# Optimization experiments

Measured on AMD Instinct MI355X. Metric: run time of the kernel, lower is better.

Reference implementation:

```python
import jax, jax.numpy as jnp
import numpy as np

# ---- static configuration (mirrors init_kwargs) ----
B, NCAM = 1, 6
FC, FH, FW = 128, 16, 44              # featureShape
ORFH, ORFW = 128, 352                 # transformedImgShape H, W
D_ST, D_END, D_STEP = 1.0, 49.0, 1.0
D = int(np.arange(D_ST, D_END, D_STEP).shape[0])   # 48 depth bins
OUTC = 128
XB = (-50.0, 50.0, 1.0)
YB = (-50.0, 50.0, 1.0)
BEV_H = int((YB[1] - YB[0]) / YB[2])  # 100
BEV_W = int((XB[1] - XB[0]) / XB[2])  # 100
THRESH = 0.05                         # opacity_filter
ERR_TOL = 1.0                         # error_tolerance
COV_DILATE = 0.3                      # 3DGS low-pass on 2D cov diagonal
ALPHA_MAX = 0.99
ALPHA_MIN = 1.0 / 255.0
BN_EPS = 1e-3


def _frustum():
    ds = jnp.arange(D_ST, D_END, D_STEP, dtype=jnp.float32)[:, None, None]
    xs = jnp.linspace(0.0, ORFW - 1.0, FW, dtype=jnp.float32)[None, None, :]
    ys = jnp.linspace(0.0, ORFH - 1.0, FH, dtype=jnp.float32)[None, :, None]
    shp = (D, FH, FW)
    return jnp.stack([jnp.broadcast_to(xs, shp), jnp.broadcast_to(ys, shp),
                      jnp.broadcast_to(ds, shp)], axis=-1)  # [D,FH,FW,3]


def _conv(x, w, b, pad):
    y = jax.lax.conv_general_dilated(x, w, (1, 1), [(pad, pad), (pad, pad)],
                                     dimension_numbers=('NCHW', 'OIHW', 'NCHW'))
    return y + b[None, :, None, None]


def _bn(x, g, beta, m, v):
    # eval-mode BatchNorm2d with running stats
    inv = g / jnp.sqrt(v + BN_EPS)
    return (x - m[None, :, None, None]) * inv[None, :, None, None] + beta[None, :, None, None]


def _rasterize(features, means, cov6, opac):
    """Differentiable BEV Gaussian splatting (alpha compositing in index order).
    features [G,C], means [G,3] (normalized to [-1,1]), cov6 [G,6]=(xx,xy,xz,yy,yz,zz), opac [G].
    """
    h, w = BEV_H, BEV_W
    sh, sw = h / 2.0, w / 2.0                 # h/FoVy, w/FoVx with FoV=2
    op = jnp.where(opac > THRESH, opac, 0.0)  # opacity cull (variable-length mask in torch)
    # full_proj_transform: row0 -> row index (y), row1 -> col index (x)
    py = h / 2.0 - sh * means[:, 1]
    px = w / 2.0 - sw * means[:, 0]
    # 2D covariance in (py,px) basis: J Sigma3 J^T with J = [[0,-sh,0],[-sw,0,0]]
    a = sh * sh * cov6[:, 3] + COV_DILATE     # var along py (from Sigma_yy)
    b = sh * sw * cov6[:, 1]                  # cov(py,px) (from Sigma_xy)
    c = sw * sw * cov6[:, 0] + COV_DILATE     # var along px (from Sigma_xx)
    det = a * c - b * b
    op = jnp.where(det > 0.0, op, 0.0)
    inv_det = 1.0 / jnp.where(det > 0.0, det, 1.0)
    ys = jnp.arange(h, dtype=jnp.float32)
    xs = jnp.arange(w, dtype=jnp.float32)
    dy = py[None, :] - ys[:, None]            # [h,G]
    dx = px[None, :] - xs[:, None]            # [w,G]
    # power = -0.5 d^T Sigma2^{-1} d, Sigma2^{-1} = [[c,-b],[-b,a]]/det
    power = (-0.5 * (c * inv_det) * dy * dy)[:, None, :] \
            + (-0.5 * (a * inv_det) * dx * dx)[None, :, :] \
            + (b * inv_det) * dy[:, None, :] * dx[None, :, :]   # [h,w,G]
    alpha = jnp.minimum(ALPHA_MAX, op * jnp.exp(jnp.minimum(power, 0.0)))
    alpha = jnp.where(alpha < ALPHA_MIN, 0.0, alpha)
    T = jnp.cumprod(1.0 - alpha, axis=-1)
    T_excl = jnp.concatenate([jnp.ones_like(T[..., :1]), T[..., :-1]], axis=-1)
    wgt = alpha * T_excl                      # [h,w,G]
    bev = jnp.einsum('hwg,gc->chw', wgt, features)   # bg color = 0
    return bev


def reference(cam2ego_rot, cam2ego_trans, cam_intrins, post_cam2ego_rot, post_cam2ego_trans,
              img_feats, conv1_w, conv1_b, bn1_g, bn1_b, bn1_m, bn1_v,
              conv2_w, conv2_b, bn2_g, bn2_b, bn2_m, bn2_v, conv3_w, conv3_b):
    # --- geometry lifting ---
    frustum = _frustum()                                             # [D,FH,FW,3]
    pts = frustum[None, None] - post_cam2ego_trans[:, :, None, None, None, :]
    pts = jnp.einsum('bnij,bndhwj->bndhwi', jnp.linalg.inv(post_cam2ego_rot), pts)
    pts = jnp.concatenate([pts[..., :2] * pts[..., 2:3], pts[..., 2:3]], axis=-1)
    combine = cam2ego_rot @ jnp.linalg.inv(cam_intrins)
    geometry = jnp.einsum('bnij,bndhwj->bndhwi', combine, pts) \
               + cam2ego_trans[:, :, None, None, None, :]            # [B,N,D,FH,FW,3]
    # --- depth net ---
    x = img_feats.reshape(B * NCAM, FC, FH, FW)
    x = jax.nn.relu(_bn(_conv(x, conv1_w, conv1_b, 1), bn1_g, bn1_b, bn1_m, bn1_v))
    x = jax.nn.relu(_bn(_conv(x, conv2_w, conv2_b, 1), bn2_g, bn2_b, bn2_m, bn2_v))
    x = _conv(x, conv3_w, conv3_b, 0)                                # [B*N, OUTC+D+1, H, W]
    depth_prob = jax.nn.softmax(x[:, :D], axis=1).reshape(B, NCAM, D, FH, FW)
    opac = jax.nn.sigmoid(x[:, D:D + 1]).reshape(B, NCAM, FH, FW)
    feats = x[:, D + 1:].reshape(B, NCAM, OUTC, FH, FW)
    # --- per-pixel Gaussian moments over the depth distribution ---
    means3d = jnp.einsum('bndhw,bndhwi->bnhwi', depth_prob, geometry)
    delta = means3d[:, :, None] - geometry                           # [B,N,D,FH,FW,3]
    cov = jnp.einsum('bndhw,bndhwi,bndhwj->bnhwij', depth_prob, delta, delta)
    cov = cov * (ERR_TOL ** 2 / 9.0)
    # --- normalize to BEV frame ---
    center = jnp.array([(XB[0] + XB[1]) / 2.0, (YB[0] + YB[1]) / 2.0, 0.0], jnp.float32)
    scale = jnp.array([2.0 / (XB[1] - XB[0]), 2.0 / (YB[1] - YB[0]), 1.0], jnp.float32)
    means_n = (means3d - center) * scale
    cov_n = cov * (scale[:, None] * scale[None, :])
    cov6 = jnp.stack([cov_n[..., 0, 0], cov_n[..., 0, 1], cov_n[..., 0, 2],
                      cov_n[..., 1, 1], cov_n[..., 1, 2], cov_n[..., 2, 2]], axis=-1)
    G = NCAM * FH * FW
    f = jnp.transpose(feats, (0, 1, 3, 4, 2)).reshape(B, G, OUTC)
    m = means_n.reshape(B, G, 3)
    c6 = cov6.reshape(B, G, 6)
    o = opac.reshape(B, G)
    bev = jax.vmap(_rasterize)(f, m, c6, o)                          # [B,OUTC,BEV_H,BEV_W]
    return bev


def setup_inputs() -> dict:
    key = jax.random.key(0)
    ks = jax.random.split(key, 16)
    eye = jnp.eye(3, dtype=jnp.float32)
    cam2ego_rot = eye + 0.05 * jax.random.normal(ks[0], (B, NCAM, 3, 3), jnp.float32)
    cam2ego_trans = 0.5 * jax.random.normal(ks[1], (B, NCAM, 3), jnp.float32)
    intr = jnp.array([[260.0, 0.0, ORFW / 2.0], [0.0, 260.0, ORFH / 2.0], [0.0, 0.0, 1.0]], jnp.float32)
    cam_intrins = jnp.broadcast_to(intr, (B, NCAM, 3, 3)) * (1.0 + 0.01 * jax.random.normal(ks[2], (B, NCAM, 1, 1), jnp.float32))
    post_cam2ego_rot = eye + 0.01 * jax.random.normal(ks[3], (B, NCAM, 3, 3), jnp.float32)
    post_cam2ego_trans = 2.0 * jax.random.normal(ks[4], (B, NCAM, 3), jnp.float32)
    img_feats = jax.random.normal(ks[5], (B, NCAM, FC, FH, FW), jnp.float32)
    def cw(k, o, i, kh, kw):
        return jax.random.normal(k, (o, i, kh, kw), jnp.float32) / np.sqrt(i * kh * kw)
    inp = dict(cam2ego_rot=cam2ego_rot, cam2ego_trans=cam2ego_trans, cam_intrins=cam_intrins,
               post_cam2ego_rot=post_cam2ego_rot, post_cam2ego_trans=post_cam2ego_trans,
               img_feats=img_feats,
               conv1_w=cw(ks[6], FC, FC, 3, 3), conv1_b=jnp.zeros((FC,), jnp.float32),
               bn1_g=jnp.ones((FC,), jnp.float32), bn1_b=0.1 * jax.random.normal(ks[7], (FC,), jnp.float32),
               bn1_m=jnp.zeros((FC,), jnp.float32), bn1_v=jnp.ones((FC,), jnp.float32),
               conv2_w=cw(ks[8], FC, FC, 3, 3), conv2_b=jnp.zeros((FC,), jnp.float32),
               bn2_g=jnp.ones((FC,), jnp.float32), bn2_b=0.1 * jax.random.normal(ks[9], (FC,), jnp.float32),
               bn2_m=jnp.zeros((FC,), jnp.float32), bn2_v=jnp.ones((FC,), jnp.float32),
               conv3_w=cw(ks[10], OUTC + D + 1, FC, 1, 1),
               conv3_b=jnp.zeros((OUTC + D + 1,), jnp.float32))
    return inp
```

## Files before the change

kernel.cpp:

```cpp
#include <hip/hip_runtime.h>
#include <math.h>

#define NCAM 6
#define FHh 16
#define FWw 44
#define PIX 704
#define FCc 128
#define DB 48
#define C3 177
#define C3PAD 192
#define KCONV 1152
#define NG 4224
#define BEVN 10000
#define CHUNK 2048
#define TH_LOG (-5.5412635f)

#define OFF_WT1    0
#define OFF_WT2    147456
#define OFF_WT3    294912
#define OFF_GEO    319488
#define OFF_X1     724992
#define OFF_X2     1265664
#define OFF_X3     1806336
#define OFF_PRM    2553984
#define OFF_PRM2   2570880
#define OFF_FEATT  2579328
#define OFF_PART   3120000

typedef __attribute__((ext_vector_type(8))) short bf16x8;
typedef __attribute__((ext_vector_type(4))) float f32x4;
typedef __attribute__((ext_vector_type(4))) int i32x4;

__device__ __forceinline__ unsigned short f2bf(float x) {
  unsigned u = __float_as_uint(x);
  return (unsigned short)((u + 0x7FFF + ((u >> 16) & 1)) >> 16);
}
__device__ __forceinline__ float bf2f(unsigned short h) {
  return __uint_as_float(((unsigned)h) << 16);
}

__device__ __forceinline__ void inv3(const float* A, float* I) {
  float a=A[0],b=A[1],c=A[2],d=A[3],e=A[4],f=A[5],g=A[6],h=A[7],i=A[8];
  float c0 = e*i - f*h, c1 = f*g - d*i, c2 = d*h - e*g;
  float det = a*c0 + b*c1 + c*c2;
  float id = 1.f/det;
  I[0]=c0*id; I[1]=(c*h-b*i)*id; I[2]=(b*f-c*e)*id;
  I[3]=c1*id; I[4]=(a*i-c*g)*id; I[5]=(c*d-a*f)*id;
  I[6]=c2*id; I[7]=(b*g-a*h)*id; I[8]=(a*e-b*d)*id;
}

__global__ void k_geom(const float* __restrict__ rot, const float* __restrict__ intr,
                       const float* __restrict__ post_rot,
                       const float* __restrict__ trans, const float* __restrict__ post_trans,
                       float* __restrict__ ws) {
  __shared__ float sm[NCAM][24];
  if (threadIdx.x < NCAM) {
    int n = threadIdx.x;
    float ip[9], ii[9];
    inv3(post_rot + n*9, ip);
    inv3(intr + n*9, ii);
    const float* R = rot + n*9;
    for (int j = 0; j < 9; ++j) sm[n][j] = ip[j];
    for (int r = 0; r < 3; ++r)
      for (int c = 0; c < 3; ++c) {
        float s = 0.f;
        for (int k = 0; k < 3; ++k) s += R[r*3+k]*ii[k*3+c];
        sm[n][9 + r*3 + c] = s;
      }
  }
  __syncthreads();
  int idx = blockIdx.x*256 + threadIdx.x;
  if (idx >= NCAM*DB*PIX) return;
  int n = idx / (DB*PIX);
  int rem = idx % (DB*PIX);
  int d = rem / PIX;
  int hw = rem % PIX;
  int h = hw / FWw, w = hw % FWw;
  float fx = w * (351.0f/43.0f);
  float fy = h * (127.0f/15.0f);
  float fz = 1.0f + (float)d;
  const float* pt = post_trans + n*3;
  float v0 = fx - pt[0], v1 = fy - pt[1], v2 = fz - pt[2];
  const float* m = sm[n];
  float x = m[0]*v0 + m[1]*v1 + m[2]*v2;
  float y = m[3]*v0 + m[4]*v1 + m[5]*v2;
  float z = m[6]*v0 + m[7]*v1 + m[8]*v2;
  float q0 = x*z, q1 = y*z, q2 = z;
  const float* c = m + 9;
  const float* t = trans + n*3;
  float gx = c[0]*q0 + c[1]*q1 + c[2]*q2 + t[0];
  float gy = c[3]*q0 + c[4]*q1 + c[5]*q2 + t[1];
  ((float2*)(ws + OFF_GEO))[idx] = make_float2(gx, gy);
}

__global__ void k_wtrans(const float* __restrict__ w1, const float* __restrict__ w2,
                         const float* __restrict__ w3, float* __restrict__ ws) {
  int e = blockIdx.x*256 + threadIdx.x;
  if (e < 147456) {
    float v1 = w1[e], v2 = w2[e];
    unsigned short h1 = f2bf(v1), h2 = f2bf(v2);
    unsigned short l1 = f2bf(v1 - bf2f(h1)), l2 = f2bf(v2 - bf2f(h2));
    unsigned short* wt1 = (unsigned short*)(ws + OFF_WT1);
    unsigned short* wt2 = (unsigned short*)(ws + OFF_WT2);
    wt1[e] = h1; wt1[147456 + e] = l1;
    wt2[e] = h2; wt2[147456 + e] = l2;
  }
  if (e < 192*128) {
    int oc = e >> 7, k = e & 127;
    float v = (oc < C3) ? w3[oc*FCc + k] : 0.f;
    unsigned short h = f2bf(v);
    unsigned short* wt3 = (unsigned short*)(ws + OFF_WT3);
    wt3[e] = h; wt3[24576 + e] = f2bf(v - bf2f(h));
  }
}

#define LROW 20

__global__ __launch_bounds__(256) void k_gemm_mfma(
    const float* __restrict__ in, const float* ws, float* __restrict__ part, int woff)
{
  __shared__ int alds[2][64*LROW];
  __shared__ int blds[2][64*LROW];
  int tid = threadIdx.x;
  int px0 = blockIdx.x * 64;
  int oc0 = blockIdx.y * 64;
  int z = blockIdx.z; int n = z >> 2, ks = z & 3;
  const unsigned short* whi = (const unsigned short*)(ws + woff);
  const unsigned short* wlo = whi + 147456;
  const float* inn = in + (size_t)n*FCc*PIX;
  int wv = tid >> 6, lane = tid & 63;
  int a_oc = tid >> 2, a_kq = tid & 3;
  int b_px = tid & 63, b_kq = tid >> 6;
  int p = px0 + b_px; int b_y = p / FWw, b_x = p - b_y*FWw;
  int k00 = ks * 288;

  i32x4 pa_h, pa_l; float bv[8];
  auto issueA = [&](int s) {
    size_t gi = (size_t)(oc0 + a_oc)*KCONV + (k00 + s*32 + a_kq*8);
    pa_h = *(const i32x4*)(whi + gi);
    pa_l = *(const i32x4*)(wlo + gi);
  };
  auto issueB = [&](int s) {
    #pragma unroll
    for (int j = 0; j < 8; ++j) {
      int k = k00 + s*32 + b_kq*8 + j;
      int ic = k / 9, tap = k - ic*9;
      int ky = tap / 3, kx = tap - ky*3;
      int yy = b_y + ky - 1, xx = b_x + kx - 1;
      float v = 0.f;
      if ((unsigned)yy < FHh && (unsigned)xx < FWw) v = inn[(size_t)ic*PIX + yy*FWw + xx];
      bv[j] = v;
    }
  };

  f32x4 a00 = {0.f,0.f,0.f,0.f}, a01 = a00, a10 = a00, a11 = a00;
  int ocr = (wv >> 1) * 32, pxr = (wv & 1) * 32;
  int dq = (lane >> 4) * 4;
  int rA0 = (ocr + (lane & 15)) * LROW + dq;
  int rA1 = rA0 + 16*LROW;
  int rB0 = (pxr + (lane & 15)) * LROW + dq;
  int rB1 = rB0 + 16*LROW;
  int aw = a_oc*LROW + a_kq*4;
  int bw = b_px*LROW + b_kq*4;

  issueA(0); issueB(0);
  for (int s = 0; s < 9; ++s) {
    __syncthreads();
    *(i32x4*)&alds[0][aw] = pa_h;
    *(i32x4*)&alds[1][aw] = pa_l;
    {
      i32x4 vh, vl;
      int th[8], tl[8];
      #pragma unroll
      for (int j = 0; j < 8; ++j) {
        unsigned short h = f2bf(bv[j]);
        th[j] = h; tl[j] = f2bf(bv[j] - bf2f(h));
      }
      vh.x = th[0]|(th[1]<<16); vh.y = th[2]|(th[3]<<16);
      vh.z = th[4]|(th[5]<<16); vh.w = th[6]|(th[7]<<16);
      vl.x = tl[0]|(tl[1]<<16); vl.y = tl[2]|(tl[3]<<16);
      vl.z = tl[4]|(tl[5]<<16); vl.w = tl[6]|(tl[7]<<16);
      *(i32x4*)&blds[0][bw] = vh;
      *(i32x4*)&blds[1][bw] = vl;
    }
    __syncthreads();
    if (s < 8) { issueA(s+1); issueB(s+1); }
    bf16x8 ah0 = *(bf16x8*)&alds[0][rA0], ah1 = *(bf16x8*)&alds[0][rA1];
    bf16x8 al0 = *(bf16x8*)&alds[1][rA0], al1 = *(bf16x8*)&alds[1][rA1];
    bf16x8 bh0 = *(bf16x8*)&blds[0][rB0], bh1 = *(bf16x8*)&blds[0][rB1];
    bf16x8 bl0 = *(bf16x8*)&blds[1][rB0], bl1 = *(bf16x8*)&blds[1][rB1];
    a00 = __builtin_amdgcn_mfma_f32_16x16x32_bf16(ah0, bh0, a00, 0, 0, 0);
    a01 = __builtin_amdgcn_mfma_f32_16x16x32_bf16(ah0, bh1, a01, 0, 0, 0);
    a10 = __builtin_amdgcn_mfma_f32_16x16x32_bf16(ah1, bh0, a10, 0, 0, 0);
    a11 = __builtin_amdgcn_mfma_f32_16x16x32_bf16(ah1, bh1, a11, 0, 0, 0);
    a00 = __builtin_amdgcn_mfma_f32_16x16x32_bf16(ah0, bl0, a00, 0, 0, 0);
    a01 = __builtin_amdgcn_mfma_f32_16x16x32_bf16(ah0, bl1, a01, 0, 0, 0);
    a10 = __builtin_amdgcn_mfma_f32_16x16x32_bf16(ah1, bl0, a10, 0, 0, 0);
    a11 = __builtin_amdgcn_mfma_f32_16x16x32_bf16(ah1, bl1, a11, 0, 0, 0);
    a00 = __builtin_amdgcn_mfma_f32_16x16x32_bf16(al0, bh0, a00, 0, 0, 0);
    a01 = __builtin_amdgcn_mfma_f32_16x16x32_bf16(al0, bh1, a01, 0, 0, 0);
    a10 = __builtin_amdgcn_mfma_f32_16x16x32_bf16(al1, bh0, a10, 0, 0, 0);
    a11 = __builtin_amdgcn_mfma_f32_16x16x32_bf16(al1, bh1, a11, 0, 0, 0);
  }
  float* pp = part + (size_t)(ks*NCAM + n)*FCc*PIX;
  int ocb = oc0 + ocr + ((lane >> 4) << 2);
  int pxb = px0 + pxr + (lane & 15);
  #pragma unroll
  for (int i = 0; i < 4; ++i) {
    pp[(size_t)(ocb + i)*PIX + pxb]           = a00[i];
    pp[(size_t)(ocb + i)*PIX + pxb + 16]      = a01[i];
    pp[(size_t)(ocb + 16 + i)*PIX + pxb]      = a10[i];
    pp[(size_t)(ocb + 16 + i)*PIX + pxb + 16] = a11[i];
  }
}

__global__ __launch_bounds__(256) void k_gemm_mfma3(
    const float* __restrict__ in, const float* ws,
    const float* __restrict__ bias, float* __restrict__ outbuf)
{
  __shared__ int alds[2][64*LROW];
  __shared__ int blds[2][64*LROW];
  int tid = threadIdx.x;
  int px0 = blockIdx.x * 64;
  int oc0 = blockIdx.y * 64;
  int n = blockIdx.z;
  const unsigned short* whi = (const unsigned short*)(ws + OFF_WT3);
  const unsigned short* wlo = whi + 24576;
  const float* inn = in + (size_t)n*FCc*PIX;
  int wv = tid >> 6, lane = tid & 63;
  int a_oc = tid >> 2, a_kq = tid & 3;
  int b_px = tid & 63, b_kq = tid >> 6;
  int p = px0 + b_px;

  i32x4 pa_h, pa_l; float bvv[8];
  auto issueA = [&](int s) {
    size_t gi = (size_t)(oc0 + a_oc)*128 + (s*32 + a_kq*8);
    pa_h = *(const i32x4*)(whi + gi);
    pa_l = *(const i32x4*)(wlo + gi);
  };
  auto issueB = [&](int s) {
    #pragma unroll
    for (int j = 0; j < 8; ++j) {
      int ic = s*32 + b_kq*8 + j;
      bvv[j] = inn[(size_t)ic*PIX + p];
    }
  };

  f32x4 a00 = {0.f,0.f,0.f,0.f}, a01 = a00, a10 = a00, a11 = a00;
  int ocr = (wv >> 1) * 32, pxr = (wv & 1) * 32;
  int dq = (lane >> 4) * 4;
  int rA0 = (ocr + (lane & 15)) * LROW + dq;
  int rA1 = rA0 + 16*LROW;
  int rB0 = (pxr + (lane & 15)) * LROW + dq;
  int rB1 = rB0 + 16*LROW;
  int aw = a_oc*LROW + a_kq*4;
  int bw = b_px*LROW + b_kq*4;

  issueA(0); issueB(0);
  for (int s = 0; s < 4; ++s) {
    __syncthreads();
    *(i32x4*)&alds[0][aw] = pa_h;
    *(i32x4*)&alds[1][aw] = pa_l;
    {
      i32x4 vh, vl;
      int th[8], tl[8];
      #pragma unroll
      for (int j = 0; j < 8; ++j) {
        unsigned short h = f2bf(bvv[j]);
        th[j] = h; tl[j] = f2bf(bvv[j] - bf2f(h));
      }
      vh.x = th[0]|(th[1]<<16); vh.y = th[2]|(th[3]<<16);
      vh.z = th[4]|(th[5]<<16); vh.w = th[6]|(th[7]<<16);
      vl.x = tl[0]|(tl[1]<<16); vl.y = tl[2]|(tl[3]<<16);
      vl.z = tl[4]|(tl[5]<<16); vl.w = tl[6]|(tl[7]<<16);
      *(i32x4*)&blds[0][bw] = vh;
      *(i32x4*)&blds[1][bw] = vl;
    }
    __syncthreads();
    if (s < 3) { issueA(s+1); issueB(s+1); }
    bf16x8 ah0 = *(bf16x8*)&alds[0][rA0], ah1 = *(bf16x8*)&alds[0][rA1];
    bf16x8 al0 = *(bf16x8*)&alds[1][rA0], al1 = *(bf16x8*)&alds[1][rA1];
    bf16x8 bh0 = *(bf16x8*)&blds[0][rB0], bh1 = *(bf16x8*)&blds[0][rB1];
    bf16x8 bl0 = *(bf16x8*)&blds[1][rB0], bl1 = *(bf16x8*)&blds[1][rB1];
    a00 = __builtin_amdgcn_mfma_f32_16x16x32_bf16(ah0, bh0, a00, 0, 0, 0);
    a01 = __builtin_amdgcn_mfma_f32_16x16x32_bf16(ah0, bh1, a01, 0, 0, 0);
    a10 = __builtin_amdgcn_mfma_f32_16x16x32_bf16(ah1, bh0, a10, 0, 0, 0);
    a11 = __builtin_amdgcn_mfma_f32_16x16x32_bf16(ah1, bh1, a11, 0, 0, 0);
    a00 = __builtin_amdgcn_mfma_f32_16x16x32_bf16(ah0, bl0, a00, 0, 0, 0);
    a01 = __builtin_amdgcn_mfma_f32_16x16x32_bf16(ah0, bl1, a01, 0, 0, 0);
    a10 = __builtin_amdgcn_mfma_f32_16x16x32_bf16(ah1, bl0, a10, 0, 0, 0);
    a11 = __builtin_amdgcn_mfma_f32_16x16x32_bf16(ah1, bl1, a11, 0, 0, 0);
    a00 = __builtin_amdgcn_mfma_f32_16x16x32_bf16(al0, bh0, a00, 0, 0, 0);
    a01 = __builtin_amdgcn_mfma_f32_16x16x32_bf16(al0, bh1, a01, 0, 0, 0);
    a10 = __builtin_amdgcn_mfma_f32_16x16x32_bf16(al1, bh0, a10, 0, 0, 0);
    a11 = __builtin_amdgcn_mfma_f32_16x16x32_bf16(al1, bh1, a11, 0, 0, 0);
  }
  int ocb = oc0 + ocr + ((lane >> 4) << 2);
  int pxb = px0 + pxr + (lane & 15);
  #pragma unroll
  for (int i = 0; i < 4; ++i) {
    int o0 = ocb + i, o1 = ocb + 16 + i;
    if (o0 < C3) {
      float b = bias[o0];
      outbuf[(size_t)(n*C3 + o0)*PIX + pxb]      = a00[i] + b;
      outbuf[(size_t)(n*C3 + o0)*PIX + pxb + 16] = a01[i] + b;
    }
    if (o1 < C3) {
      float b = bias[o1];
      outbuf[(size_t)(n*C3 + o1)*PIX + pxb]      = a10[i] + b;
      outbuf[(size_t)(n*C3 + o1)*PIX + pxb + 16] = a11[i] + b;
    }
  }
}

__global__ void k_epi_bn(const float* __restrict__ part, const float* __restrict__ cb,
                         const float* __restrict__ g, const float* __restrict__ be,
                         const float* __restrict__ mn, const float* __restrict__ vr,
                         float* __restrict__ out, int KSPLIT)
{
  int idx = blockIdx.x*256 + threadIdx.x;
  if (idx >= NCAM*FCc*176) return;
  int px4 = idx % 176;
  int t = idx / 176;
  int oc = t % FCc;
  int n = t / FCc;
  float4 s = {0.f,0.f,0.f,0.f};
  for (int ks = 0; ks < KSPLIT; ++ks) {
    const float4* p = (const float4*)(part + (size_t)((ks*NCAM+n)*FCc + oc)*PIX);
    float4 v = p[px4];
    s.x += v.x; s.y += v.y; s.z += v.z; s.w += v.w;
  }
  float inv = g[oc] * rsqrtf(vr[oc] + 1e-3f);
  float sh = (cb[oc] - mn[oc]) * inv + be[oc];
  float4 o;
  o.x = fmaxf(s.x*inv + sh, 0.f);
  o.y = fmaxf(s.y*inv + sh, 0.f);
  o.z = fmaxf(s.z*inv + sh, 0.f);
  o.w = fmaxf(s.w*inv + sh, 0.f);
  ((float4*)(out + (size_t)(n*FCc + oc)*PIX))[px4] = o;
}

__global__ void k_moments(float* __restrict__ ws) {
  int wid  = (blockIdx.x * 256 + threadIdx.x) >> 6;
  int lane = threadIdx.x & 63;
  int n = wid / PIX, hw = wid % PIX;
  const float* x3 = ws + OFF_X3 + (size_t)n*C3*PIX + hw;
  float logit = (lane < DB) ? x3[(size_t)lane*PIX] : -1e30f;
  float mx = logit;
  for (int off = 1; off < 64; off <<= 1) mx = fmaxf(mx, __shfl_xor(mx, off));
  float e = (lane < DB) ? expf(logit - mx) : 0.f;
  float s = e;
  for (int off = 1; off < 64; off <<= 1) s += __shfl_xor(s, off);
  float p = e / s;
  float gx = 0.f, gy = 0.f;
  if (lane < DB) {
    float2 g2 = ((const float2*)(ws + OFF_GEO))[(size_t)(n*DB + lane)*PIX + hw];
    gx = g2.x; gy = g2.y;
  }
  float sx = p*gx;
  for (int off = 1; off < 64; off <<= 1) sx += __shfl_xor(sx, off);
  float sy = p*gy;
  for (int off = 1; off < 64; off <<= 1) sy += __shfl_xor(sy, off);
  float dx = gx - sx, dy = gy - sy;
  float c00 = p*dx*dx, c01 = p*dx*dy, c11 = p*dy*dy;
  for (int off = 1; off < 64; off <<= 1) c00 += __shfl_xor(c00, off);
  for (int off = 1; off < 64; off <<= 1) c01 += __shfl_xor(c01, off);
  for (int off = 1; off < 64; off <<= 1) c11 += __shfl_xor(c11, off);
  float opl = x3[(size_t)DB*PIX];
  float opac = 1.f / (1.f + expf(-opl));
  float a = c11*(1.f/9.f) + 0.3f;
  float b = c01*(1.f/9.f);
  float c = c00*(1.f/9.f) + 0.3f;
  float py = 50.f - sy;
  float px = 50.f - sx;
  float det = a*c - b*b;
  float op = (opac > 0.05f) ? opac : 0.f;
  float invd = 1.f;
  if (det > 0.f) invd = 1.f/det; else op = 0.f;
  if (lane == 0) {
    float lop = (op > 0.f) ? logf(op) : -1e30f;
    ((float4*)(ws + OFF_PRM))[wid]  = make_float4(py, px, -0.5f*c*invd, -0.5f*a*invd);
    ((float2*)(ws + OFF_PRM2))[wid] = make_float2(b*invd, lop);
  }
  float* ft = ws + OFF_FEATT + (size_t)wid*128;
  ft[lane]      = x3[(size_t)(DB + 1 + lane)*PIX];
  ft[lane + 64] = x3[(size_t)(DB + 1 + lane + 64)*PIX];
}

template<int CTRL, int RMASK>
__device__ __forceinline__ float dpp_mul(float v) {
  int t = __builtin_amdgcn_update_dpp(0x3f800000, __float_as_int(v), CTRL, RMASK, 0xF, false);
  return v * __int_as_float(t);
}

__global__ __launch_bounds__(512) void k_raster(const float* __restrict__ ws,
                                                float* __restrict__ out) {
  __shared__ float4 s4[CHUNK];
  __shared__ float2 s2[CHUNK];
  int lane = threadIdx.x & 63, wv = threadIdx.x >> 6;
  int pix = blockIdx.x * 8 + wv;
  float yi = (float)(pix / 100), xi = (float)(pix % 100);
  const float4* prm4 = (const float4*)(ws + OFF_PRM);
  const float2* prm2 = (const float2*)(ws + OFF_PRM2);
  const float2* ft = (const float2*)(ws + OFF_FEATT);
  float T = 1.f, ax = 0.f, ay = 0.f;
  bool alive = true;
  for (int c0 = 0; c0 < NG; c0 += CHUNK) {
    if (__syncthreads_count(alive ? 1 : 0) == 0) break;
    int cn = min(CHUNK, NG - c0);
    for (int i = threadIdx.x; i < cn; i += 512) {
      s4[i] = prm4[c0 + i];
      s2[i] = prm2[c0 + i];
    }
    __syncthreads();
    if (alive) {
      for (int gl = 0; gl < cn; gl += 64) {
        float4 c4 = s4[gl + lane];
        float2 c2 = s2[gl + lane];
        float dyv = c4.x - yi, dxv = c4.y - xi;
        float pw = c4.z*dyv*dyv + c4.w*dxv*dxv + c2.x*dyv*dxv;
        float t  = pw + c2.y;
        bool hit = (t >= TH_LOG);
        unsigned long long m0 = __ballot(hit);
        if (m0) {
          float alpha = __expf(fminf(t, c2.y));
          alpha = fminf(alpha, 0.99f);
          alpha = hit ? alpha : 0.f;
          float P = 1.f - alpha;
          P = dpp_mul<0x111, 0xF>(P);
          P = dpp_mul<0x112, 0xF>(P);
          P = dpp_mul<0x114, 0xF>(P);
          P = dpp_mul<0x118, 0xF>(P);
          P = dpp_mul<0x142, 0xA>(P);
          P = dpp_mul<0x143, 0xC>(P);
          float E = __int_as_float(__builtin_amdgcn_update_dpp(
                      0x3f800000, __float_as_int(P), 0x138, 0xF, 0xF, false));
          float w = alpha * T * E;
          T *= __int_as_float(__builtin_amdgcn_readlane(__float_as_int(P), 63));
          unsigned long long mask = __ballot(w > 1e-9f);
          int g0 = c0 + gl;
          while (mask) {
            int jj[8];
            #pragma unroll
            for (int b = 0; b < 8; ++b) {
              if (mask) { jj[b] = __builtin_ctzll(mask); mask &= mask - 1ull; }
              else jj[b] = -1;
            }
            float2 fb[8]; float wb[8];
            #pragma unroll
            for (int b = 0; b < 8; ++b) {
              int j = (jj[b] >= 0) ? jj[b] : jj[0];
              fb[b] = ft[(size_t)(g0 + j)*64 + lane];
              wb[b] = (jj[b] >= 0)
                ? __int_as_float(__builtin_amdgcn_readlane(__float_as_int(w), jj[b]))
                : 0.f;
            }
            #pragma unroll
            for (int b = 0; b < 8; ++b) { ax += wb[b]*fb[b].x; ay += wb[b]*fb[b].y; }
          }
          if (T < 1e-7f) { alive = false; break; }
        }
      }
    }
  }
  out[(size_t)(2*lane)*BEVN + pix]   = ax;
  out[(size_t)(2*lane+1)*BEVN + pix] = ay;
}

extern "C" void kernel_launch(void* const* d_in, const int* in_sizes, int n_in,
                              void* d_out, int out_size, void* d_ws, size_t ws_size,
                              hipStream_t stream) {
  const float* rot        = (const float*)d_in[0];
  const float* trans      = (const float*)d_in[1];
  const float* intr       = (const float*)d_in[2];
  const float* post_rot   = (const float*)d_in[3];
  const float* post_trans = (const float*)d_in[4];
  const float* img        = (const float*)d_in[5];
  const float* w1  = (const float*)d_in[6];
  const float* b1  = (const float*)d_in[7];
  const float* g1  = (const float*)d_in[8];
  const float* be1 = (const float*)d_in[9];
  const float* m1  = (const float*)d_in[10];
  const float* v1  = (const float*)d_in[11];
  const float* w2  = (const float*)d_in[12];
  const float* b2  = (const float*)d_in[13];
  const float* g2  = (const float*)d_in[14];
  const float* be2 = (const float*)d_in[15];
  const float* m2  = (const float*)d_in[16];
  const float* v2  = (const float*)d_in[17];
  const float* w3  = (const float*)d_in[18];
  const float* b3  = (const float*)d_in[19];
  float* ws  = (float*)d_ws;
  float* out = (float*)d_out;

  k_wtrans<<<576, 256, 0, stream>>>(w1, w2, w3, ws);
  k_geom<<<792, 256, 0, stream>>>(rot, intr, post_rot, trans, post_trans, ws);

  k_gemm_mfma<<<dim3(11,2,24), 256, 0, stream>>>(img, ws, ws+OFF_PART, OFF_WT1);
  k_epi_bn<<<528, 256, 0, stream>>>(ws+OFF_PART, b1, g1, be1, m1, v1, ws+OFF_X1, 4);
  k_gemm_mfma<<<dim3(11,2,24), 256, 0, stream>>>(ws+OFF_X1, ws, ws+OFF_PART, OFF_WT2);
  k_epi_bn<<<528, 256, 0, stream>>>(ws+OFF_PART, b2, g2, be2, m2, v2, ws+OFF_X2, 4);
  k_gemm_mfma3<<<dim3(11,3,6), 256, 0, stream>>>(ws+OFF_X2, ws, b3, ws+OFF_X3);

  k_moments<<<1056, 256, 0, stream>>>(ws);
  k_raster<<<1250, 512, 0, stream>>>(ws, out);
}
```

Before: 124.5 us.

## Split Gaussian rasterization across three depth segments and combine with transmittance

The rasterizer now splits the 4224 Gaussians into three contiguous segments, each handled by its own block per pixel group, writing partial color and final transmittance to workspace. A new combine kernel composites the three partials front-to-back, weighting later segments by the product of earlier transmittances. This triples the number of blocks to fill the GPU and shortens each block's serial compositing loop. In exchange it loses early termination across segments, adds an extra kernel launch and workspace traffic, and relocates the workspace buffers so the split outputs overlay earlier-stage data.

```diff
diff --git a/kernel.cpp b/kernel.cpp
--- a/kernel.cpp
+++ b/kernel.cpp
@@ -12,7 +12,8 @@
 #define KCONV 1152
 #define NG 4224
 #define BEVN 10000
-#define CHUNK 2048
+#define NSPLIT 3
+#define SG 1408
 #define TH_LOG (-5.5412635f)
 
 #define OFF_WT1    0
@@ -22,10 +23,12 @@
 #define OFF_X1     724992
 #define OFF_X2     1265664
 #define OFF_X3     1806336
-#define OFF_PRM    2553984
-#define OFF_PRM2   2570880
-#define OFF_FEATT  2579328
-#define OFF_PART   3120000
+#define OFF_PART   2553984
+#define OFF_PRM    4716672
+#define OFF_PRM2   4733568
+#define OFF_FEATT  4742016
+#define OFF_SF     0
+#define OFF_SP     3840000
 
 typedef __attribute__((ext_vector_type(8))) short bf16x8;
 typedef __attribute__((ext_vector_type(4))) float f32x4;
@@ -394,77 +397,92 @@
 }
 
 __global__ __launch_bounds__(512) void k_raster(const float* __restrict__ ws,
-                                                float* __restrict__ out) {
-  __shared__ float4 s4[CHUNK];
-  __shared__ float2 s2[CHUNK];
+                                                float* __restrict__ wsout) {
+  __shared__ float4 s4[SG];
+  __shared__ float2 s2[SG];
+  int lane = threadIdx.x & 63, wv = threadIdx.x >> 6;
+  int split = blockIdx.x / 1250;
+  int pxb   = blockIdx.x % 1250;
+  int pix = pxb * 8 + wv;
+  float yi = (float)(pix / 100), xi = (float)(pix % 100);
+  int gbase = split * SG;
+  const float4* prm4 = (const float4*)(ws + OFF_PRM) + gbase;
+  const float2* prm2 = (const float2*)(ws + OFF_PRM2) + gbase;
+  const float2* ft = (const float2*)(ws + OFF_FEATT);
+  for (int i = threadIdx.x; i < SG; i += 512) {
+    s4[i] = prm4[i];
+    s2[i] = prm2[i];
+  }
+  __syncthreads();
+  float T = 1.f, ax = 0.f, ay = 0.f;
+  for (int gl = 0; gl < SG; gl += 64) {
+    float4 c4 = s4[gl + lane];
+    float2 c2 = s2[gl + lane];
+    float dyv = c4.x - yi, dxv = c4.y - xi;
+    float pw = c4.z*dyv*dyv + c4.w*dxv*dxv + c2.x*dyv*dxv;
+    float t  = pw + c2.y;
+    bool hit = (t >= TH_LOG);
+    unsigned long long m0 = __ballot(hit);
+    if (m0) {
+      float alpha = __expf(fminf(t, c2.y));
+      alpha = fminf(alpha, 0.99f);
+      alpha = hit ? alpha : 0.f;
+      float P = 1.f - alpha;
+      P = dpp_mul<0x111, 0xF>(P);
+      P = dpp_mul<0x112, 0xF>(P);
+      P = dpp_mul<0x114, 0xF>(P);
+      P = dpp_mul<0x118, 0xF>(P);
+      P = dpp_mul<0x142, 0xA>(P);
+      P = dpp_mul<0x143, 0xC>(P);
+      float E = __int_as_float(__builtin_amdgcn_update_dpp(
+                  0x3f800000, __float_as_int(P), 0x138, 0xF, 0xF, false));
+      float w = alpha * T * E;
+      T *= __int_as_float(__builtin_amdgcn_readlane(__float_as_int(P), 63));
+      unsigned long long mask = __ballot(w > 1e-9f);
+      int g0 = gbase + gl;
+      while (mask) {
+        int jj[8];
+        #pragma unroll
+        for (int b = 0; b < 8; ++b) {
+          if (mask) { jj[b] = __builtin_ctzll(mask); mask &= mask - 1ull; }
+          else jj[b] = -1;
+        }
+        float2 fb[8]; float wb[8];
+        #pragma unroll
+        for (int b = 0; b < 8; ++b) {
+          int j = (jj[b] >= 0) ? jj[b] : jj[0];
+          fb[b] = ft[(size_t)(g0 + j)*64 + lane];
+          wb[b] = (jj[b] >= 0)
+            ? __int_as_float(__builtin_amdgcn_readlane(__float_as_int(w), jj[b]))
+            : 0.f;
+        }
+        #pragma unroll
+        for (int b = 0; b < 8; ++b) { ax += wb[b]*fb[b].x; ay += wb[b]*fb[b].y; }
+      }
+      if (T < 1e-7f) break;
+    }
+  }
+  float* sf = wsout + OFF_SF + ((size_t)split*BEVN + pix)*128;
+  sf[2*lane]   = ax;
+  sf[2*lane+1] = ay;
+  if (lane == 0) (wsout + OFF_SP)[split*BEVN + pix] = T;
+}
+
+__global__ __launch_bounds__(512) void k_combine(const float* __restrict__ ws,
+                                                 float* __restrict__ out) {
   int lane = threadIdx.x & 63, wv = threadIdx.x >> 6;
   int pix = blockIdx.x * 8 + wv;
-  float yi = (float)(pix / 100), xi = (float)(pix % 100);
-  const float4* prm4 = (const float4*)(ws + OFF_PRM);
-  const float2* prm2 = (const float2*)(ws + OFF_PRM2);
-  const float2* ft = (const float2*)(ws + OFF_FEATT);
-  float T = 1.f, ax = 0.f, ay = 0.f;
-  bool alive = true;
-  for (int c0 = 0; c0 < NG; c0 += CHUNK) {
-    if (__syncthreads_count(alive ? 1 : 0) == 0) break;
-    int cn = min(CHUNK, NG - c0);
-    for (int i = threadIdx.x; i < cn; i += 512) {
-      s4[i] = prm4[c0 + i];
-      s2[i] = prm2[c0 + i];
-    }
-    __syncthreads();
-    if (alive) {
-      for (int gl = 0; gl < cn; gl += 64) {
-        float4 c4 = s4[gl + lane];
-        float2 c2 = s2[gl + lane];
-        float dyv = c4.x - yi, dxv = c4.y - xi;
-        float pw = c4.z*dyv*dyv + c4.w*dxv*dxv + c2.x*dyv*dxv;
-        float t  = pw + c2.y;
-        bool hit = (t >= TH_LOG);
-        unsigned long long m0 = __ballot(hit);
-        if (m0) {
-          float alpha = __expf(fminf(t, c2.y));
-          alpha = fminf(alpha, 0.99f);
-          alpha = hit ? alpha : 0.f;
-          float P = 1.f - alpha;
-          P = dpp_mul<0x111, 0xF>(P);
-          P = dpp_mul<0x112, 0xF>(P);
-          P = dpp_mul<0x114, 0xF>(P);
-          P = dpp_mul<0x118, 0xF>(P);
-          P = dpp_mul<0x142, 0xA>(P);
-          P = dpp_mul<0x143, 0xC>(P);
-          float E = __int_as_float(__builtin_amdgcn_update_dpp(
-                      0x3f800000, __float_as_int(P), 0x138, 0xF, 0xF, false));
-          float w = alpha * T * E;
-          T *= __int_as_float(__builtin_amdgcn_readlane(__float_as_int(P), 63));
-          unsigned long long mask = __ballot(w > 1e-9f);
-          int g0 = c0 + gl;
-          while (mask) {
-            int jj[8];
-            #pragma unroll
-            for (int b = 0; b < 8; ++b) {
-              if (mask) { jj[b] = __builtin_ctzll(mask); mask &= mask - 1ull; }
-              else jj[b] = -1;
-            }
-            float2 fb[8]; float wb[8];
-            #pragma unroll
-            for (int b = 0; b < 8; ++b) {
-              int j = (jj[b] >= 0) ? jj[b] : jj[0];
-              fb[b] = ft[(size_t)(g0 + j)*64 + lane];
-              wb[b] = (jj[b] >= 0)
-                ? __int_as_float(__builtin_amdgcn_readlane(__float_as_int(w), jj[b]))
-                : 0.f;
-            }
-            #pragma unroll
-            for (int b = 0; b < 8; ++b) { ax += wb[b]*fb[b].x; ay += wb[b]*fb[b].y; }
-          }
-          if (T < 1e-7f) { alive = false; break; }
-        }
-      }
-    }
-  }
-  out[(size_t)(2*lane)*BEVN + pix]   = ax;
-  out[(size_t)(2*lane+1)*BEVN + pix] = ay;
+  const float* sp = ws + OFF_SP;
+  float P0 = sp[pix], P1 = sp[BEVN + pix];
+  const float2* f0 = (const float2*)(ws + OFF_SF + (size_t)pix*128);
+  const float2* f1 = (const float2*)(ws + OFF_SF + ((size_t)BEVN + pix)*128);
+  const float2* f2 = (const float2*)(ws + OFF_SF + ((size_t)2*BEVN + pix)*128);
+  float2 a = f0[lane], b = f1[lane], c = f2[lane];
+  float w1 = P0, w2 = P0*P1;
+  float ox = a.x + w1*b.x + w2*c.x;
+  float oy = a.y + w1*b.y + w2*c.y;
+  out[(size_t)(2*lane)*BEVN + pix]   = ox;
+  out[(size_t)(2*lane+1)*BEVN + pix] = oy;
 }
 
 extern "C" void kernel_launch(void* const* d_in, const int* in_sizes, int n_in,
@@ -503,5 +521,6 @@
   k_gemm_mfma3<<<dim3(11,3,6), 256, 0, stream>>>(ws+OFF_X2, ws, b3, ws+OFF_X3);
 
   k_moments<<<1056, 256, 0, stream>>>(ws);
-  k_raster<<<1250, 512, 0, stream>>>(ws, out);
-}
+  k_raster<<<3750, 512, 0, stream>>>(ws, ws);
+  k_combine<<<1250, 512, 0, stream>>>(ws, out);
+}
```

New measurement: 123.4 us. No clear change (-0.9%).
